# Kernel optimization log

Measured on AMD Instinct MI355X. Metric: run time of the kernel, lower is better.

The kernel has to match this reference:

```python
import jax, jax.numpy as jnp
import numpy as np

B, S, I, D = 1, 128, 256, 64   # batch, n_seq, n_res, n_feat
P, DO = 32, 128                # n_feat_proj, n_feat_out


def setup_inputs() -> dict:
    key = jax.random.key(0)
    ks = jax.random.split(key, 7)
    M = jax.random.normal(ks[0], (B, S, I, D), dtype=jnp.float32)
    # LayerNorm params
    ln_gamma = jnp.ones((D,), dtype=jnp.float32)
    ln_beta = jnp.zeros((D,), dtype=jnp.float32)
    # projections (torch Linear: y = x @ W.T + b)
    Wa = jax.random.normal(ks[1], (P, D), dtype=jnp.float32) * (1.0 / np.sqrt(D))
    ba = jnp.zeros((P,), dtype=jnp.float32)
    Wb = jax.random.normal(ks[2], (P, D), dtype=jnp.float32) * (1.0 / np.sqrt(D))
    bb = jnp.zeros((P,), dtype=jnp.float32)
    # output projection (init 'zero' falls through to default init in the source;
    # use small random weights so the reference output is non-trivial)
    Wo = jax.random.normal(ks[3], (DO, P * P), dtype=jnp.float32) * (1.0 / np.sqrt(P * P))
    bo = jnp.zeros((DO,), dtype=jnp.float32)
    return {"M": M, "ln_gamma": ln_gamma, "ln_beta": ln_beta,
            "Wa": Wa, "ba": ba, "Wb": Wb, "bb": bb, "Wo": Wo, "bo": bo}


def _layernorm(x, gamma, beta, eps=1e-5):
    mu = jnp.mean(x, axis=-1, keepdims=True)
    var = jnp.mean(jnp.square(x - mu), axis=-1, keepdims=True)
    return (x - mu) * jax.lax.rsqrt(var + eps) * gamma + beta


def reference(M, ln_gamma, ln_beta, Wa, ba, Wb, bb, Wo, bo):
    Mn = _layernorm(M, ln_gamma, ln_beta)            # (b,s,i,d)
    left = jnp.einsum('bsid,pd->bsip', Mn, Wa) + ba  # (b,s,i,P)
    right = jnp.einsum('bsjd,qd->bsjq', Mn, Wb) + bb # (b,s,j,P)
    # outer-product contraction over the sequence dim
    O = jnp.einsum('bsid,bsje->bijde', left, right)  # (b,i,j,P,P)
    O = O.reshape(O.shape[0], O.shape[1], O.shape[2], -1)  # (b,i,j,P*P)
    Z = jnp.einsum('bijk,ok->bijo', O, Wo) + bo      # (b,i,j,DO)
    return Z
```

## Files before the change

### kernel.cpp

```cpp
#include <hip/hip_runtime.h>

typedef __attribute__((ext_vector_type(4))) float          f32x4;
typedef __attribute__((ext_vector_type(8))) short          bf16x8;
typedef __attribute__((ext_vector_type(4))) unsigned short u16x4;
typedef __attribute__((ext_vector_type(8))) unsigned short u16x8;

__device__ __forceinline__ unsigned short f2bf(float f) {
  union { float f; unsigned u; } v; v.f = f;
  unsigned r = v.u + 0x7fffu + ((v.u >> 16) & 1u);
  return (unsigned short)(r >> 16);
}

__device__ __forceinline__ void gload_lds16(const void* g, void* l) {
  __builtin_amdgcn_global_load_lds(
      (const __attribute__((address_space(1))) unsigned int*)g,
      (__attribute__((address_space(3))) unsigned int*)l, 16, 0, 0);
}

#define S_  128
#define I_  256
#define D_  64
#define P_  32
#define DO_ 128

__global__ __launch_bounds__(256) void ln_proj(
    const float* __restrict__ M,  const float* __restrict__ gamma,
    const float* __restrict__ beta,
    const float* __restrict__ Wa, const float* __restrict__ ba,
    const float* __restrict__ Wb, const float* __restrict__ bb,
    const float* __restrict__ Wo,
    unsigned short* __restrict__ LtT, unsigned short* __restrict__ RtT,
    unsigned short* __restrict__ WoP)
{
  __shared__ __align__(16) float mnAll[32 * 68];
  __shared__ __align__(16) float lsm[32 * 33];
  __shared__ __align__(16) float rsm[32 * 33];

  const int tid  = threadIdx.x;
  const int lane = tid & 63;
  const int w    = tid >> 6;
  const int i    = blockIdx.x >> 2;
  const int sq   = blockIdx.x & 3;

  const float g  = gamma[lane];
  const float be = beta[lane];
  #pragma unroll
  for (int u = 0; u < 8; ++u) {
    int s_loc = w * 8 + u;
    int s     = sq * 32 + s_loc;
    float x = M[(s * I_ + i) * D_ + lane];
    float s1 = x, s2 = x * x;
    #pragma unroll
    for (int m = 1; m < 64; m <<= 1) {
      s1 += __shfl_xor(s1, m, 64);
      s2 += __shfl_xor(s2, m, 64);
    }
    float mean = s1 * (1.0f / 64.0f);
    float var  = s2 * (1.0f / 64.0f) - mean * mean;
    mnAll[s_loc * 68 + lane] = (x - mean) * rsqrtf(var + 1e-5f) * g + be;
  }
  __syncthreads();

  {
    const int p    = lane & 31;
    const int side = lane >> 5;
    const float* wrow = (side ? Wb : Wa) + p * D_;
    const float  bias = side ? bb[p] : ba[p];
    f32x4 wv[16];
    #pragma unroll
    for (int c = 0; c < 16; ++c) wv[c] = *(const f32x4*)(wrow + c * 4);
    float* dst = side ? rsm : lsm;
    #pragma unroll
    for (int u = 0; u < 8; ++u) {
      int s_loc = w * 8 + u;
      float acc = bias;
      #pragma unroll
      for (int c = 0; c < 16; ++c) {
        f32x4 m4 = *(const f32x4*)(&mnAll[s_loc * 68 + c * 4]);
        acc += m4.x * wv[c].x + m4.y * wv[c].y + m4.z * wv[c].z + m4.w * wv[c].w;
      }
      dst[s_loc * 33 + p] = acc;
    }
  }
  __syncthreads();

  {
    int arr = tid >> 7;
    int p   = (tid >> 2) & 31;
    int c   = tid & 3;
    int s0  = c * 8;
    const float* src = arr ? rsm : lsm;
    unsigned short* dstg = (arr ? RtT : LtT) + (i * 32 + p) * S_ + sq * 32 + s0;
    u16x8 v;
    #pragma unroll
    for (int k = 0; k < 8; ++k) v[k] = f2bf(src[(s0 + k) * 33 + p]);
    *(u16x8*)dstg = v;
  }

  if (blockIdx.x < 512) {
    int f = (int)blockIdx.x * 256 + tid;
    int o = f >> 10, kp = f & 1023, q = kp >> 5, p = kp & 31;
    WoP[f] = f2bf(Wo[o * 1024 + p * 32 + q]);
  }
}

__global__ __launch_bounds__(512, 2) void fused_gemm(
    const unsigned short* __restrict__ LtT,
    const unsigned short* __restrict__ RtT,
    const unsigned short* __restrict__ WoP,
    const float* __restrict__ bo,
    float* __restrict__ Z)
{
  __shared__ __align__(16) unsigned short ldsmem[73728];
  char* Lc  = (char*)ldsmem;
  char* LtS = Lc;
  char* RtS = Lc + 65536;
  char* WoS = Lc + 81920;
  char* Osh = Lc + 114688;

  const int tid  = threadIdx.x;
  const int lane = tid & 63;
  const int wid  = tid >> 6;
  const int l15  = lane & 15;
  const int l4   = lane >> 4;

  const int bid = ((int)blockIdx.x & 7) * 32 + ((int)blockIdx.x >> 3);
  const int bi  = bid >> 3;
  const int bjp = bid & 7;

  {
    const char* g = (const char*)LtT + (unsigned)bi * 65536u;
    #pragma unroll
    for (int t2 = 0; t2 < 8; ++t2) {
      int t = wid + t2 * 8;
      unsigned off = (unsigned)t * 1024u;
      unsigned y = off + (unsigned)lane * 16u;
      unsigned r = y >> 8, cb = y & 255u;
      gload_lds16(g + r * 256u + (cb ^ ((r & 7u) << 4)), LtS + off);
    }
  }

  const int wm = wid >> 2;
  const int wn = wid & 3;

  float bov[2];
  #pragma unroll
  for (int n_i = 0; n_i < 2; ++n_i) bov[n_i] = bo[(wn * 2 + n_i) * 16 + l15];

  f32x4 zacc[4][2];
  #pragma unroll
  for (int a = 0; a < 4; ++a)
    #pragma unroll
    for (int b = 0; b < 2; ++b) { f32x4 zz = {0.f,0.f,0.f,0.f}; zacc[a][b] = zz; }

  bf16x8 af[4][2];

  for (int jj = 0; jj < 2; ++jj) {
    const int bj = bjp + jj * 8;

    #pragma unroll
    for (int t2 = 0; t2 < 2; ++t2) {
      int t = wid + t2 * 8;
      unsigned off = (unsigned)t * 1024u;
      unsigned y = off + (unsigned)lane * 16u;
      unsigned lr = y >> 8, cb = y & 255u;
      unsigned grow = (unsigned)bj * 512u + (lr >> 2) * 32u + 0u * 4u + (lr & 3u);
      gload_lds16((const char*)RtT + grow * 256u + (cb ^ ((lr & 7u) << 4)), RtS + off);
    }
    #pragma unroll
    for (int t2 = 0; t2 < 4; ++t2) {
      int t = wid + t2 * 8;
      unsigned off = (unsigned)t * 1024u;
      unsigned y = off + (unsigned)lane * 16u;
      unsigned o = y >> 8, cb = y & 255u;
      gload_lds16((const char*)WoP + o * 2048u + 0u * 256u + (cb ^ ((o & 7u) << 4)), WoS + off);
    }

    if (jj == 1) {
      const int bjo = bjp;
      #pragma unroll
      for (int m_i = 0; m_i < 4; ++m_i)
        #pragma unroll
        for (int r = 0; r < 4; ++r) {
          int pair = (wm * 4 + m_i) * 16 + l4 * 4 + r;
          int i_loc = pair >> 4, j_loc = pair & 15;
          float* zrow = Z + (((bi * 8 + i_loc) * I_) + (bjo * 16 + j_loc)) * DO_;
          #pragma unroll
          for (int n_i = 0; n_i < 2; ++n_i)
            zrow[(wn * 2 + n_i) * 16 + l15] = zacc[m_i][n_i][r] + bov[n_i];
        }
      #pragma unroll
      for (int a = 0; a < 4; ++a)
        #pragma unroll
        for (int b = 0; b < 2; ++b) { f32x4 zz = {0.f,0.f,0.f,0.f}; zacc[a][b] = zz; }
    }

    __syncthreads();

    if (jj == 0) {
      #pragma unroll
      for (int kk = 0; kk < 4; ++kk)
        #pragma unroll
        for (int ai = 0; ai < 2; ++ai) {
          unsigned r = (unsigned)((wid * 2 + ai) * 16 + l15);
          af[kk][ai] = *(const bf16x8*)(LtS + r * 256u +
                         (((unsigned)(kk * 64 + l4 * 16)) ^ ((r & 7u) << 4)));
        }
    }

    for (int c = 0; c < 8; ++c) {
      f32x4 acc[2][4];
      #pragma unroll
      for (int a = 0; a < 2; ++a)
        #pragma unroll
        for (int b = 0; b < 4; ++b) { f32x4 zz = {0.f,0.f,0.f,0.f}; acc[a][b] = zz; }

      #pragma unroll
      for (int kk = 0; kk < 4; ++kk) {
        bf16x8 bfr[4];
        #pragma unroll
        for (int bt = 0; bt < 4; ++bt) {
          unsigned r = (unsigned)(bt * 16 + l15);
          bfr[bt] = *(const bf16x8*)(RtS + r * 256u +
                      (((unsigned)(kk * 64 + l4 * 16)) ^ ((r & 7u) << 4)));
        }
        #pragma unroll
        for (int ai = 0; ai < 2; ++ai)
          #pragma unroll
          for (int bt = 0; bt < 4; ++bt)
            acc[ai][bt] = __builtin_amdgcn_mfma_f32_16x16x32_bf16(
                af[kk][ai], bfr[bt], acc[ai][bt], 0, 0, 0);
      }

      #pragma unroll
      for (int ai = 0; ai < 2; ++ai) {
        int at = wid * 2 + ai;
        unsigned prhi = (unsigned)(at >> 1) * 16u;
        unsigned p0   = (unsigned)((at & 1) * 16 + l4 * 4);
        #pragma unroll
        for (int bt = 0; bt < 4; ++bt) {
          unsigned pair = prhi + (unsigned)(bt * 4) + ((unsigned)l15 >> 2);
          unsigned cb   = ((unsigned)l15 & 3u) * 64u + p0 * 2u;
          u16x4 v;
          v.x = f2bf(acc[ai][bt][0]);
          v.y = f2bf(acc[ai][bt][1]);
          v.z = f2bf(acc[ai][bt][2]);
          v.w = f2bf(acc[ai][bt][3]);
          *(u16x4*)(Osh + pair * 256u + (cb ^ ((pair & 7u) << 4))) = v;
        }
      }

      __syncthreads();

      if (c < 7) {
        #pragma unroll
        for (int t2 = 0; t2 < 2; ++t2) {
          int t = wid + t2 * 8;
          unsigned off = (unsigned)t * 1024u;
          unsigned y = off + (unsigned)lane * 16u;
          unsigned lr = y >> 8, cb = y & 255u;
          unsigned grow = (unsigned)bj * 512u + (lr >> 2) * 32u +
                          (unsigned)(c + 1) * 4u + (lr & 3u);
          gload_lds16((const char*)RtT + grow * 256u + (cb ^ ((lr & 7u) << 4)),
                      RtS + off);
        }
      }

      #pragma unroll
      for (int kk2 = 0; kk2 < 4; ++kk2) {
        bf16x8 afr[4], wbr[2];
        #pragma unroll
        for (int m_i = 0; m_i < 4; ++m_i) {
          unsigned r = (unsigned)((wm * 4 + m_i) * 16 + l15);
          afr[m_i] = *(const bf16x8*)(Osh + r * 256u +
                       (((unsigned)(kk2 * 64 + l4 * 16)) ^ ((r & 7u) << 4)));
        }
        #pragma unroll
        for (int n_i = 0; n_i < 2; ++n_i) {
          unsigned r = (unsigned)((wn * 2 + n_i) * 16 + l15);
          wbr[n_i] = *(const bf16x8*)(WoS + r * 256u +
                       (((unsigned)(kk2 * 64 + l4 * 16)) ^ ((r & 7u) << 4)));
        }
        #pragma unroll
        for (int m_i = 0; m_i < 4; ++m_i)
          #pragma unroll
          for (int n_i = 0; n_i < 2; ++n_i)
            zacc[m_i][n_i] = __builtin_amdgcn_mfma_f32_16x16x32_bf16(
                afr[m_i], wbr[n_i], zacc[m_i][n_i], 0, 0, 0);
      }

      __syncthreads();

      if (c < 7) {
        #pragma unroll
        for (int t2 = 0; t2 < 4; ++t2) {
          int t = wid + t2 * 8;
          unsigned off = (unsigned)t * 1024u;
          unsigned y = off + (unsigned)lane * 16u;
          unsigned o = y >> 8, cb = y & 255u;
          gload_lds16((const char*)WoP + o * 2048u + (unsigned)(c + 1) * 256u +
                      (cb ^ ((o & 7u) << 4)), WoS + off);
        }
      }
    }
  }

  {
    const int bjo = bjp + 8;
    #pragma unroll
    for (int m_i = 0; m_i < 4; ++m_i)
      #pragma unroll
      for (int r = 0; r < 4; ++r) {
        int pair = (wm * 4 + m_i) * 16 + l4 * 4 + r;
        int i_loc = pair >> 4, j_loc = pair & 15;
        float* zrow = Z + (((bi * 8 + i_loc) * I_) + (bjo * 16 + j_loc)) * DO_;
        #pragma unroll
        for (int n_i = 0; n_i < 2; ++n_i)
          zrow[(wn * 2 + n_i) * 16 + l15] = zacc[m_i][n_i][r] + bov[n_i];
      }
  }
}

extern "C" void kernel_launch(void* const* d_in, const int* in_sizes, int n_in,
                              void* d_out, int out_size, void* d_ws, size_t ws_size,
                              hipStream_t stream) {
  const float* M     = (const float*)d_in[0];
  const float* gamma = (const float*)d_in[1];
  const float* beta  = (const float*)d_in[2];
  const float* Wa    = (const float*)d_in[3];
  const float* ba    = (const float*)d_in[4];
  const float* Wb    = (const float*)d_in[5];
  const float* bb    = (const float*)d_in[6];
  const float* Wo    = (const float*)d_in[7];
  const float* bo    = (const float*)d_in[8];
  float* Z = (float*)d_out;

  unsigned short* LtT = (unsigned short*)d_ws;
  unsigned short* RtT = LtT + 1048576;
  unsigned short* WoP = RtT + 1048576;

  ln_proj<<<1024, 256, 0, stream>>>(M, gamma, beta, Wa, ba, Wb, bb, Wo,
                                    LtT, RtT, WoP);
  fused_gemm<<<256, 512, 0, stream>>>(LtT, RtT, WoP, bo, Z);
}
```

Baseline: 126.2 us.

## Split fused GEMM blocks to one j-tile each, drop LDS staging of left operand

Each block now handles a single (bi, bj) tile instead of two j-tiles, which doubles the grid to 512 blocks. The left-operand fragments are loaded straight from global memory into registers rather than staged through LDS. This cuts LDS per block from 144KB to 80KB and raises the launch-bounds occupancy hint from 2 to 4. The aim is more resident blocks and better latency hiding. In exchange, the left tile is reloaded once per j-tile, the first-stage accumulators are split into two halves to save registers, and the mapping of blocks to tiles changes.

```diff
diff --git a/kernel.cpp b/kernel.cpp
--- a/kernel.cpp
+++ b/kernel.cpp
@@ -104,19 +104,18 @@
   }
 }
 
-__global__ __launch_bounds__(512, 2) void fused_gemm(
+__global__ __launch_bounds__(512, 4) void fused_gemm(
     const unsigned short* __restrict__ LtT,
     const unsigned short* __restrict__ RtT,
     const unsigned short* __restrict__ WoP,
     const float* __restrict__ bo,
     float* __restrict__ Z)
 {
-  __shared__ __align__(16) unsigned short ldsmem[73728];
+  __shared__ __align__(16) unsigned short ldsmem[40960];
   char* Lc  = (char*)ldsmem;
-  char* LtS = Lc;
-  char* RtS = Lc + 65536;
-  char* WoS = Lc + 81920;
-  char* Osh = Lc + 114688;
+  char* RtS = Lc;
+  char* WoS = Lc + 16384;
+  char* Osh = Lc + 49152;
 
   const int tid  = threadIdx.x;
   const int lane = tid & 63;
@@ -124,21 +123,36 @@
   const int l15  = lane & 15;
   const int l4   = lane >> 4;
 
-  const int bid = ((int)blockIdx.x & 7) * 32 + ((int)blockIdx.x >> 3);
-  const int bi  = bid >> 3;
-  const int bjp = bid & 7;
-
-  {
-    const char* g = (const char*)LtT + (unsigned)bi * 65536u;
-    #pragma unroll
-    for (int t2 = 0; t2 < 8; ++t2) {
-      int t = wid + t2 * 8;
-      unsigned off = (unsigned)t * 1024u;
-      unsigned y = off + (unsigned)lane * 16u;
-      unsigned r = y >> 8, cb = y & 255u;
-      gload_lds16(g + r * 256u + (cb ^ ((r & 7u) << 4)), LtS + off);
-    }
-  }
+  const int bid = ((int)blockIdx.x & 7) * 64 + ((int)blockIdx.x >> 3);
+  const int bi  = bid >> 4;
+  const int bj  = bid & 15;
+
+  #pragma unroll
+  for (int t2 = 0; t2 < 2; ++t2) {
+    int t = wid + t2 * 8;
+    unsigned off = (unsigned)t * 1024u;
+    unsigned y = off + (unsigned)lane * 16u;
+    unsigned lr = y >> 8, cb = y & 255u;
+    unsigned grow = (unsigned)bj * 512u + (lr >> 2) * 32u + (lr & 3u);
+    gload_lds16((const char*)RtT + grow * 256u + (cb ^ ((lr & 7u) << 4)), RtS + off);
+  }
+  #pragma unroll
+  for (int t2 = 0; t2 < 4; ++t2) {
+    int t = wid + t2 * 8;
+    unsigned off = (unsigned)t * 1024u;
+    unsigned y = off + (unsigned)lane * 16u;
+    unsigned o = y >> 8, cb = y & 255u;
+    gload_lds16((const char*)WoP + o * 2048u + (cb ^ ((o & 7u) << 4)), WoS + off);
+  }
+
+  bf16x8 af[4][2];
+  #pragma unroll
+  for (int kk = 0; kk < 4; ++kk)
+    #pragma unroll
+    for (int ai = 0; ai < 2; ++ai) {
+      unsigned rg = (unsigned)(bi * 256 + (wid * 2 + ai) * 16 + l15);
+      af[kk][ai] = *(const bf16x8*)(LtT + rg * 128u + (unsigned)(kk * 32 + l4 * 8));
+    }
 
   const int wm = wid >> 2;
   const int wn = wid & 3;
@@ -153,172 +167,119 @@
     #pragma unroll
     for (int b = 0; b < 2; ++b) { f32x4 zz = {0.f,0.f,0.f,0.f}; zacc[a][b] = zz; }
 
-  bf16x8 af[4][2];
-
-  for (int jj = 0; jj < 2; ++jj) {
-    const int bj = bjp + jj * 8;
-
-    #pragma unroll
-    for (int t2 = 0; t2 < 2; ++t2) {
-      int t = wid + t2 * 8;
-      unsigned off = (unsigned)t * 1024u;
-      unsigned y = off + (unsigned)lane * 16u;
-      unsigned lr = y >> 8, cb = y & 255u;
-      unsigned grow = (unsigned)bj * 512u + (lr >> 2) * 32u + 0u * 4u + (lr & 3u);
-      gload_lds16((const char*)RtT + grow * 256u + (cb ^ ((lr & 7u) << 4)), RtS + off);
-    }
-    #pragma unroll
-    for (int t2 = 0; t2 < 4; ++t2) {
-      int t = wid + t2 * 8;
-      unsigned off = (unsigned)t * 1024u;
-      unsigned y = off + (unsigned)lane * 16u;
-      unsigned o = y >> 8, cb = y & 255u;
-      gload_lds16((const char*)WoP + o * 2048u + 0u * 256u + (cb ^ ((o & 7u) << 4)), WoS + off);
-    }
-
-    if (jj == 1) {
-      const int bjo = bjp;
-      #pragma unroll
-      for (int m_i = 0; m_i < 4; ++m_i)
-        #pragma unroll
-        for (int r = 0; r < 4; ++r) {
-          int pair = (wm * 4 + m_i) * 16 + l4 * 4 + r;
-          int i_loc = pair >> 4, j_loc = pair & 15;
-          float* zrow = Z + (((bi * 8 + i_loc) * I_) + (bjo * 16 + j_loc)) * DO_;
-          #pragma unroll
-          for (int n_i = 0; n_i < 2; ++n_i)
-            zrow[(wn * 2 + n_i) * 16 + l15] = zacc[m_i][n_i][r] + bov[n_i];
-        }
-      #pragma unroll
-      for (int a = 0; a < 4; ++a)
-        #pragma unroll
-        for (int b = 0; b < 2; ++b) { f32x4 zz = {0.f,0.f,0.f,0.f}; zacc[a][b] = zz; }
-    }
-
-    __syncthreads();
-
-    if (jj == 0) {
-      #pragma unroll
-      for (int kk = 0; kk < 4; ++kk)
-        #pragma unroll
-        for (int ai = 0; ai < 2; ++ai) {
-          unsigned r = (unsigned)((wid * 2 + ai) * 16 + l15);
-          af[kk][ai] = *(const bf16x8*)(LtS + r * 256u +
-                         (((unsigned)(kk * 64 + l4 * 16)) ^ ((r & 7u) << 4)));
-        }
-    }
-
-    for (int c = 0; c < 8; ++c) {
-      f32x4 acc[2][4];
+  __syncthreads();
+
+  for (int c = 0; c < 8; ++c) {
+    #pragma unroll
+    for (int bh = 0; bh < 2; ++bh) {
+      f32x4 acc[2][2];
       #pragma unroll
       for (int a = 0; a < 2; ++a)
         #pragma unroll
-        for (int b = 0; b < 4; ++b) { f32x4 zz = {0.f,0.f,0.f,0.f}; acc[a][b] = zz; }
+        for (int b = 0; b < 2; ++b) { f32x4 zz = {0.f,0.f,0.f,0.f}; acc[a][b] = zz; }
 
       #pragma unroll
       for (int kk = 0; kk < 4; ++kk) {
-        bf16x8 bfr[4];
-        #pragma unroll
-        for (int bt = 0; bt < 4; ++bt) {
-          unsigned r = (unsigned)(bt * 16 + l15);
-          bfr[bt] = *(const bf16x8*)(RtS + r * 256u +
+        bf16x8 bfr[2];
+        #pragma unroll
+        for (int b2 = 0; b2 < 2; ++b2) {
+          unsigned r = (unsigned)((bh * 2 + b2) * 16 + l15);
+          bfr[b2] = *(const bf16x8*)(RtS + r * 256u +
                       (((unsigned)(kk * 64 + l4 * 16)) ^ ((r & 7u) << 4)));
         }
         #pragma unroll
         for (int ai = 0; ai < 2; ++ai)
           #pragma unroll
-          for (int bt = 0; bt < 4; ++bt)
-            acc[ai][bt] = __builtin_amdgcn_mfma_f32_16x16x32_bf16(
-                af[kk][ai], bfr[bt], acc[ai][bt], 0, 0, 0);
+          for (int b2 = 0; b2 < 2; ++b2)
+            acc[ai][b2] = __builtin_amdgcn_mfma_f32_16x16x32_bf16(
+                af[kk][ai], bfr[b2], acc[ai][b2], 0, 0, 0);
       }
 
       #pragma unroll
       for (int ai = 0; ai < 2; ++ai) {
         int at = wid * 2 + ai;
-        unsigned prhi = (unsigned)(at >> 1) * 16u;
-        unsigned p0   = (unsigned)((at & 1) * 16 + l4 * 4);
-        #pragma unroll
-        for (int bt = 0; bt < 4; ++bt) {
-          unsigned pair = prhi + (unsigned)(bt * 4) + ((unsigned)l15 >> 2);
-          unsigned cb   = ((unsigned)l15 & 3u) * 64u + p0 * 2u;
+        unsigned ihi = (unsigned)(at >> 1) * 16u;
+        unsigned p0  = (unsigned)((at & 1) * 16 + l4 * 4);
+        #pragma unroll
+        for (int b2 = 0; b2 < 2; ++b2) {
+          unsigned n = (unsigned)((bh * 2 + b2) * 16 + l15);
+          unsigned pair = ihi + (n >> 2);
+          unsigned cb   = (n & 3u) * 64u + p0 * 2u;
           u16x4 v;
-          v.x = f2bf(acc[ai][bt][0]);
-          v.y = f2bf(acc[ai][bt][1]);
-          v.z = f2bf(acc[ai][bt][2]);
-          v.w = f2bf(acc[ai][bt][3]);
+          v.x = f2bf(acc[ai][b2][0]);
+          v.y = f2bf(acc[ai][b2][1]);
+          v.z = f2bf(acc[ai][b2][2]);
+          v.w = f2bf(acc[ai][b2][3]);
           *(u16x4*)(Osh + pair * 256u + (cb ^ ((pair & 7u) << 4))) = v;
         }
       }
-
-      __syncthreads();
-
-      if (c < 7) {
-        #pragma unroll
-        for (int t2 = 0; t2 < 2; ++t2) {
-          int t = wid + t2 * 8;
-          unsigned off = (unsigned)t * 1024u;
-          unsigned y = off + (unsigned)lane * 16u;
-          unsigned lr = y >> 8, cb = y & 255u;
-          unsigned grow = (unsigned)bj * 512u + (lr >> 2) * 32u +
-                          (unsigned)(c + 1) * 4u + (lr & 3u);
-          gload_lds16((const char*)RtT + grow * 256u + (cb ^ ((lr & 7u) << 4)),
-                      RtS + off);
-        }
-      }
-
-      #pragma unroll
-      for (int kk2 = 0; kk2 < 4; ++kk2) {
-        bf16x8 afr[4], wbr[2];
-        #pragma unroll
-        for (int m_i = 0; m_i < 4; ++m_i) {
-          unsigned r = (unsigned)((wm * 4 + m_i) * 16 + l15);
-          afr[m_i] = *(const bf16x8*)(Osh + r * 256u +
-                       (((unsigned)(kk2 * 64 + l4 * 16)) ^ ((r & 7u) << 4)));
-        }
-        #pragma unroll
-        for (int n_i = 0; n_i < 2; ++n_i) {
-          unsigned r = (unsigned)((wn * 2 + n_i) * 16 + l15);
-          wbr[n_i] = *(const bf16x8*)(WoS + r * 256u +
-                       (((unsigned)(kk2 * 64 + l4 * 16)) ^ ((r & 7u) << 4)));
-        }
-        #pragma unroll
-        for (int m_i = 0; m_i < 4; ++m_i)
-          #pragma unroll
-          for (int n_i = 0; n_i < 2; ++n_i)
-            zacc[m_i][n_i] = __builtin_amdgcn_mfma_f32_16x16x32_bf16(
-                afr[m_i], wbr[n_i], zacc[m_i][n_i], 0, 0, 0);
-      }
-
-      __syncthreads();
-
-      if (c < 7) {
-        #pragma unroll
-        for (int t2 = 0; t2 < 4; ++t2) {
-          int t = wid + t2 * 8;
-          unsigned off = (unsigned)t * 1024u;
-          unsigned y = off + (unsigned)lane * 16u;
-          unsigned o = y >> 8, cb = y & 255u;
-          gload_lds16((const char*)WoP + o * 2048u + (unsigned)(c + 1) * 256u +
-                      (cb ^ ((o & 7u) << 4)), WoS + off);
-        }
-      }
-    }
-  }
-
-  {
-    const int bjo = bjp + 8;
-    #pragma unroll
-    for (int m_i = 0; m_i < 4; ++m_i)
-      #pragma unroll
-      for (int r = 0; r < 4; ++r) {
-        int pair = (wm * 4 + m_i) * 16 + l4 * 4 + r;
-        int i_loc = pair >> 4, j_loc = pair & 15;
-        float* zrow = Z + (((bi * 8 + i_loc) * I_) + (bjo * 16 + j_loc)) * DO_;
+    }
+
+    __syncthreads();
+
+    if (c < 7) {
+      #pragma unroll
+      for (int t2 = 0; t2 < 2; ++t2) {
+        int t = wid + t2 * 8;
+        unsigned off = (unsigned)t * 1024u;
+        unsigned y = off + (unsigned)lane * 16u;
+        unsigned lr = y >> 8, cb = y & 255u;
+        unsigned grow = (unsigned)bj * 512u + (lr >> 2) * 32u +
+                        (unsigned)(c + 1) * 4u + (lr & 3u);
+        gload_lds16((const char*)RtT + grow * 256u + (cb ^ ((lr & 7u) << 4)),
+                    RtS + off);
+      }
+    }
+
+    #pragma unroll
+    for (int kk2 = 0; kk2 < 4; ++kk2) {
+      bf16x8 afr[4], wbr[2];
+      #pragma unroll
+      for (int m_i = 0; m_i < 4; ++m_i) {
+        unsigned r = (unsigned)((wm * 4 + m_i) * 16 + l15);
+        afr[m_i] = *(const bf16x8*)(Osh + r * 256u +
+                     (((unsigned)(kk2 * 64 + l4 * 16)) ^ ((r & 7u) << 4)));
+      }
+      #pragma unroll
+      for (int n_i = 0; n_i < 2; ++n_i) {
+        unsigned r = (unsigned)((wn * 2 + n_i) * 16 + l15);
+        wbr[n_i] = *(const bf16x8*)(WoS + r * 256u +
+                     (((unsigned)(kk2 * 64 + l4 * 16)) ^ ((r & 7u) << 4)));
+      }
+      #pragma unroll
+      for (int m_i = 0; m_i < 4; ++m_i)
         #pragma unroll
         for (int n_i = 0; n_i < 2; ++n_i)
-          zrow[(wn * 2 + n_i) * 16 + l15] = zacc[m_i][n_i][r] + bov[n_i];
-      }
-  }
+          zacc[m_i][n_i] = __builtin_amdgcn_mfma_f32_16x16x32_bf16(
+              afr[m_i], wbr[n_i], zacc[m_i][n_i], 0, 0, 0);
+    }
+
+    __syncthreads();
+
+    if (c < 7) {
+      #pragma unroll
+      for (int t2 = 0; t2 < 4; ++t2) {
+        int t = wid + t2 * 8;
+        unsigned off = (unsigned)t * 1024u;
+        unsigned y = off + (unsigned)lane * 16u;
+        unsigned o = y >> 8, cb = y & 255u;
+        gload_lds16((const char*)WoP + o * 2048u + (unsigned)(c + 1) * 256u +
+                    (cb ^ ((o & 7u) << 4)), WoS + off);
+      }
+    }
+  }
+
+  #pragma unroll
+  for (int m_i = 0; m_i < 4; ++m_i)
+    #pragma unroll
+    for (int r = 0; r < 4; ++r) {
+      int pair = (wm * 4 + m_i) * 16 + l4 * 4 + r;
+      int i_loc = pair >> 4, j_loc = pair & 15;
+      float* zrow = Z + (((bi * 8 + i_loc) * I_) + (bj * 16 + j_loc)) * DO_;
+      #pragma unroll
+      for (int n_i = 0; n_i < 2; ++n_i)
+        zrow[(wn * 2 + n_i) * 16 + l15] = zacc[m_i][n_i][r] + bov[n_i];
+    }
 }
 
 extern "C" void kernel_launch(void* const* d_in, const int* in_sizes, int n_in,
@@ -341,5 +302,5 @@
 
   ln_proj<<<1024, 256, 0, stream>>>(M, gamma, beta, Wa, ba, Wb, bb, Wo,
                                     LtT, RtT, WoP);
-  fused_gemm<<<256, 512, 0, stream>>>(LtT, RtT, WoP, bo, Z);
-}
+  fused_gemm<<<512, 512, 0, stream>>>(LtT, RtT, WoP, bo, Z);
+}
```

New measurement: 129.3 us. 1.02x slower.
